# Performance work log

Measured on AMD Instinct MI355X. Metric: run time of the kernel, lower is better.

Reference implementation:

```python
import jax, jax.numpy as jnp
import numpy as np

MODEL_DIM = 1024
NUM_HEADS = 16
HEAD_DIM = MODEL_DIM // NUM_HEADS
BATCH = 2
SEQ = 2048


def setup_inputs() -> dict:
    key = jax.random.key(0)
    k1, k2, k3 = jax.random.split(key, 3)
    scale = 1.0 / np.sqrt(MODEL_DIM)
    return {
        "embeddings": jax.random.normal(k1, (BATCH, SEQ, MODEL_DIM), dtype=jnp.float32),
        "w_qkv": jax.random.normal(k2, (MODEL_DIM, 3 * MODEL_DIM), dtype=jnp.float32) * scale,
        "b_qkv": jnp.zeros((3 * MODEL_DIM,), dtype=jnp.float32),
        "w_out": jax.random.normal(k3, (MODEL_DIM, MODEL_DIM), dtype=jnp.float32) * scale,
        "b_out": jnp.zeros((MODEL_DIM,), dtype=jnp.float32),
    }


def reference(embeddings, w_qkv, b_qkv, w_out, b_out):
    B, S, _ = embeddings.shape
    # fused QKV projection: [B, S, 3*model_dim]
    qkv = embeddings @ w_qkv + b_qkv
    # -> [B, H, S, 3*head_dim], then split
    qkv = qkv.reshape(B, S, NUM_HEADS, 3 * HEAD_DIM).transpose(0, 2, 1, 3)
    q, k, v = jnp.split(qkv, 3, axis=-1)
    # scaled dot-product attention (full O(S^2) matrix, as in original)
    scale = 1.0 / jnp.sqrt(jnp.asarray(HEAD_DIM, dtype=embeddings.dtype))
    scores = jnp.einsum("bhqd,bhkd->bhqk", q, k) * scale
    attn = jax.nn.softmax(scores, axis=-1)
    ctx = jnp.einsum("bhqk,bhkd->bhqd", attn, v)
    # merge heads -> [B, S, model_dim], output projection
    ctx = ctx.transpose(0, 2, 1, 3).reshape(B, S, NUM_HEADS * HEAD_DIM)
    return ctx @ w_out + b_out
```

## Files before the change

kernel.cpp:

```cpp
#include <hip/hip_runtime.h>
#include <hip/hip_bf16.h>

#define MODEL 1024
#define NHEADS 16
#define HDIM 64
#define BATCH 2
#define SEQ 2048
#define NROWS (BATCH*SEQ)
#define QKVN (3*MODEL)
#define QSCALE 0.1803368801111204f

typedef __bf16 bf16x8 __attribute__((ext_vector_type(8)));
typedef float f32x4 __attribute__((ext_vector_type(4)));
typedef float f32x16 __attribute__((ext_vector_type(16)));

#define GLDS(g, l) __builtin_amdgcn_global_load_lds( \
    (const __attribute__((address_space(1))) void*)(g), \
    (__attribute__((address_space(3))) void*)(l), 16, 0, 0)

__device__ inline unsigned cvtpk(float lo, float hi) {
    unsigned r;
    asm("v_cvt_pk_bf16_f32 %0, %1, %2" : "=v"(r) : "v"(lo), "v"(hi));
    return r;
}

__device__ inline size_t qk_fidx(int s, int d) {
    return (((size_t)((s >> 6) * 8 + ((s >> 5) & 1) * 4 + (d >> 4)) * 64)
            + (s & 31) + ((d >> 3) & 1) * 32) * 8 + (d & 7);
}
__device__ inline size_t v_fidx(int s, int d) {
    return (((size_t)((s >> 6) * 8 + (d >> 5) * 4 + ((s >> 4) & 3)) * 64)
            + (d & 31) + ((s >> 3) & 1) * 32) * 8 + (s & 7);
}


__global__ __launch_bounds__(256) void prep_kernel(
    const float* __restrict__ emb, __hip_bfloat16* __restrict__ Xb,
    const float* __restrict__ wqkv, __hip_bfloat16* __restrict__ Wqkvt,
    const float* __restrict__ wout, __hip_bfloat16* __restrict__ Woutt)
{
    __shared__ float tile[32][33];
    int bid = blockIdx.x, tid = threadIdx.x;
    if (bid < 4096) {
        int i = (bid * 256 + tid) * 4;
        float4 v = *(const float4*)(emb + i);
        Xb[i + 0] = __float2bfloat16(v.x);
        Xb[i + 1] = __float2bfloat16(v.y);
        Xb[i + 2] = __float2bfloat16(v.z);
        Xb[i + 3] = __float2bfloat16(v.w);
        return;
    }
    const float* in; __hip_bfloat16* out; int K, N, n0, k0;
    if (bid < 7168) {
        int t = bid - 4096; in = wqkv; out = Wqkvt; K = MODEL; N = QKVN;
        n0 = (t % 96) * 32; k0 = (t / 96) * 32;
    } else {
        int t = bid - 7168; in = wout; out = Woutt; K = MODEL; N = MODEL;
        n0 = (t & 31) * 32; k0 = (t >> 5) * 32;
    }
    int tx = tid & 31, ty = tid >> 5;
#pragma unroll
    for (int i = 0; i < 4; ++i)
        tile[ty + i * 8][tx] = in[(size_t)(k0 + ty + i * 8) * N + n0 + tx];
    __syncthreads();
#pragma unroll
    for (int i = 0; i < 4; ++i)
        out[(size_t)(n0 + ty + i * 8) * K + k0 + tx] = __float2bfloat16(tile[tx][ty + i * 8]);
}


template<int EPI>
__global__ __launch_bounds__(256) void gemm_bt_kernel(
    const __hip_bfloat16* __restrict__ A, const __hip_bfloat16* __restrict__ Bt,
    const float* __restrict__ bias, float* __restrict__ Cf,
    __hip_bfloat16* __restrict__ qb, __hip_bfloat16* __restrict__ kb,
    __hip_bfloat16* __restrict__ vb, int M, int N, int K)
{
    __shared__ __hip_bfloat16 As[128 * 32];
    __shared__ __hip_bfloat16 Bs[128 * 32];
    int tid = threadIdx.x;
    int lane = tid & 63, wv = tid >> 6;
    int wm = wv >> 1, wn = wv & 1;
    int g = lane >> 4, li = lane & 15;
    int row0 = blockIdx.y * 128, col0 = blockIdx.x * 128;

    f32x4 acc[4][4] = {};

    for (int kt = 0; kt < K; kt += 32) {
        __syncthreads();
#pragma unroll
        for (int s = 0; s < 2; ++s) {
            int idx = (s * 256 + tid) * 8;
            int r = idx >> 5, c = idx & 31;
            const __hip_bfloat16* ga = A + (size_t)(row0 + r) * K + kt + c;
            char* la = (char*)As + (size_t)(s * 4 + wv) * 1024;
            GLDS(ga, la);
            const __hip_bfloat16* gb = Bt + (size_t)(col0 + r) * K + kt + c;
            char* lb = (char*)Bs + (size_t)(s * 4 + wv) * 1024;
            GLDS(gb, lb);
        }
        __syncthreads();
        bf16x8 a[4], b[4];
#pragma unroll
        for (int m = 0; m < 4; ++m)
            a[m] = *(const bf16x8*)((const char*)As + (size_t)((wm * 64 + m * 16 + li) * 32 + g * 8) * 2);
#pragma unroll
        for (int n = 0; n < 4; ++n)
            b[n] = *(const bf16x8*)((const char*)Bs + (size_t)((wn * 64 + n * 16 + li) * 32 + g * 8) * 2);
#pragma unroll
        for (int m = 0; m < 4; ++m)
#pragma unroll
            for (int n = 0; n < 4; ++n)
                acc[m][n] = __builtin_amdgcn_mfma_f32_16x16x32_bf16(a[m], b[n], acc[m][n], 0, 0, 0);
    }

    if (EPI == 1) {
#pragma unroll
        for (int m = 0; m < 4; ++m) {
            int row = row0 + wm * 64 + m * 16 + g * 4;
#pragma unroll
            for (int n = 0; n < 4; ++n) {
                int col = col0 + wn * 64 + n * 16 + li;
                float bv = bias[col];
#pragma unroll
                for (int r = 0; r < 4; ++r)
                    Cf[(size_t)(row + r) * N + col] = acc[m][n][r] + bv;
            }
        }
    } else {
#pragma unroll
        for (int m = 0; m < 4; ++m)
#pragma unroll
            for (int r = 0; r < 4; ++r) {
                int row = row0 + wm * 64 + m * 16 + g * 4 + r;
                int b = row >> 11, s = row & 2047;
#pragma unroll
                for (int n = 0; n < 4; ++n) {
                    int col = col0 + wn * 64 + n * 16 + li;
                    float val = acc[m][n][r] + bias[col];
                    int h = col / 192;
                    int rem = col - h * 192;
                    int t = rem >> 6, d = rem & 63;
                    size_t base = (size_t)(b * NHEADS + h) * (SEQ * HDIM);
                    if (t == 0)
                        qb[base + qk_fidx(s, d)] = __float2bfloat16(val * QSCALE);
                    else if (t == 1)
                        kb[base + qk_fidx(s, d)] = __float2bfloat16(val);
                    else
                        vb[base + v_fidx(s, d)] = __float2bfloat16(val);
                }
            }
    }
}


__global__ __launch_bounds__(256, 4) void attn_kernel(
    const __hip_bfloat16* __restrict__ qfb, const __hip_bfloat16* __restrict__ kfb,
    const __hip_bfloat16* __restrict__ vfb, __hip_bfloat16* __restrict__ ctx)
{
    __shared__ float Ms[2][64], Ls[2][64], Os[2][32][64];
    int tid = threadIdx.x;
    int lane = tid & 63, w = tid >> 6;
    int qg = w & 1, kvh = w >> 1;
    int qi = lane & 31, hi = lane >> 5;
    int bh = blockIdx.x;
    int b = bh >> 4, h = bh & 15;
    int q0 = blockIdx.y * 64 + qg * 32;

    const bf16x8* QF = (const bf16x8*)qfb + (size_t)bh * 16384;
    const bf16x8* KF = (const bf16x8*)kfb + (size_t)bh * 16384;
    const bf16x8* VF = (const bf16x8*)vfb + (size_t)bh * 16384;

    bf16x8 qv[4];
#pragma unroll
    for (int st = 0; st < 4; ++st)
        qv[st] = QF[(size_t)blockIdx.y * 512 + (qg * 4 + st) * 64 + lane];

    f32x16 o0 = {}, o1 = {};
    float m = -INFINITY, l = 0.f;

    bf16x8 kc[4], kn[4];
    {
        int t32 = kvh * 32, t64 = t32 >> 1, rh = t32 & 1;
#pragma unroll
        for (int st = 0; st < 4; ++st)
            kc[st] = KF[(size_t)t64 * 512 + (rh * 4 + st) * 64 + lane];
    }

    for (int tt = 0; tt < 32; ++tt) {
        int t32 = kvh * 32 + tt;
        int t64 = t32 >> 1, rh = t32 & 1;
        __builtin_amdgcn_s_barrier();

        f32x16 s = {};
#pragma unroll
        for (int st = 0; st < 4; ++st)
            s = __builtin_amdgcn_mfma_f32_32x32x16_bf16(kc[st], qv[st], s, 0, 0, 0);

        bf16x8 vv[4];
#pragma unroll
        for (int dr = 0; dr < 2; ++dr)
#pragma unroll
            for (int ksl = 0; ksl < 2; ++ksl)
                vv[dr * 2 + ksl] = VF[(size_t)t64 * 512 + (dr * 4 + rh * 2 + ksl) * 64 + lane];
        {
            int tp = (tt < 31) ? t32 + 1 : t32;
            int p64 = tp >> 1, ph = tp & 1;
#pragma unroll
            for (int st = 0; st < 4; ++st)
                kn[st] = KF[(size_t)p64 * 512 + (ph * 4 + st) * 64 + lane];
        }

        float tm[8];
#pragma unroll
        for (int i = 0; i < 8; ++i) tm[i] = fmaxf(s[i], s[8 + i]);
#pragma unroll
        for (int i = 0; i < 4; ++i) tm[i] = fmaxf(tm[i], tm[4 + i]);
        float mx = fmaxf(fmaxf(tm[0], tm[1]), fmaxf(tm[2], tm[3]));
        mx = fmaxf(mx, __shfl_xor(mx, 32));
        if (__any(mx - m > 8.0f)) {
            float mn = fmaxf(m, mx);
            float al = __builtin_amdgcn_exp2f(m - mn);
            m = mn;
            l *= al;
#pragma unroll
            for (int i = 0; i < 16; ++i) { o0[i] *= al; o1[i] *= al; }
        }
#pragma unroll
        for (int i = 0; i < 16; ++i) s[i] = __builtin_amdgcn_exp2f(s[i] - m);
        float ts[8];
#pragma unroll
        for (int i = 0; i < 8; ++i) ts[i] = s[i] + s[8 + i];
#pragma unroll
        for (int i = 0; i < 4; ++i) ts[i] = ts[i] + ts[4 + i];
        float sum = (ts[0] + ts[1]) + (ts[2] + ts[3]);
        sum += __shfl_xor(sum, 32);
        l += sum;

        bf16x8 pb[2];
#pragma unroll
        for (int ksl = 0; ksl < 2; ++ksl) {
            const int base = ksl * 8;
            unsigned t0 = cvtpk(s[base + 0], s[base + 1]);
            unsigned t1 = cvtpk(s[base + 2], s[base + 3]);
            unsigned u0 = cvtpk(s[base + 4], s[base + 5]);
            unsigned u1 = cvtpk(s[base + 6], s[base + 7]);
            unsigned ra = __shfl_xor(hi ? t0 : u0, 32);
            unsigned rb = __shfl_xor(hi ? t1 : u1, 32);
            union { unsigned u[4]; bf16x8 v; } pk;
            pk.u[0] = hi ? ra : t0;
            pk.u[1] = hi ? rb : t1;
            pk.u[2] = hi ? u0 : ra;
            pk.u[3] = hi ? u1 : rb;
            pb[ksl] = pk.v;
        }

        o0 = __builtin_amdgcn_mfma_f32_32x32x16_bf16(vv[0], pb[0], o0, 0, 0, 0);
        o0 = __builtin_amdgcn_mfma_f32_32x32x16_bf16(vv[1], pb[1], o0, 0, 0, 0);
        o1 = __builtin_amdgcn_mfma_f32_32x32x16_bf16(vv[2], pb[0], o1, 0, 0, 0);
        o1 = __builtin_amdgcn_mfma_f32_32x32x16_bf16(vv[3], pb[1], o1, 0, 0, 0);

#pragma unroll
        for (int st = 0; st < 4; ++st) kc[st] = kn[st];
    }

    __syncthreads();
    if (kvh == 1) {
        Ms[qg][lane] = m; Ls[qg][lane] = l;
#pragma unroll
        for (int i = 0; i < 16; ++i) { Os[qg][i][lane] = o0[i]; Os[qg][16 + i][lane] = o1[i]; }
    }
    __syncthreads();
    if (kvh == 0) {
        float m2 = Ms[qg][lane], l2 = Ls[qg][lane];
        float mn = fmaxf(m, m2);
        float a = __builtin_amdgcn_exp2f(m - mn);
        float b2 = __builtin_amdgcn_exp2f(m2 - mn);
        float linv = 1.f / (l * a + l2 * b2);
        __hip_bfloat16* crow = ctx + ((size_t)(b * SEQ) + q0 + qi) * MODEL + h * HDIM;
#pragma unroll
        for (int rg = 0; rg < 4; ++rg) {
            float c0[4], c1[4];
#pragma unroll
            for (int e = 0; e < 4; ++e) {
                int i = rg * 4 + e;
                c0[e] = (o0[i] * a + Os[qg][i][lane] * b2) * linv;
                c1[e] = (o1[i] * a + Os[qg][16 + i][lane] * b2) * linv;
            }
            uint2 pk0, pk1;
            pk0.x = cvtpk(c0[0], c0[1]); pk0.y = cvtpk(c0[2], c0[3]);
            pk1.x = cvtpk(c1[0], c1[1]); pk1.y = cvtpk(c1[2], c1[3]);
            *(uint2*)(crow + rg * 8 + hi * 4) = pk0;
            *(uint2*)(crow + 32 + rg * 8 + hi * 4) = pk1;
        }
    }
}


extern "C" void kernel_launch(void* const* d_in, const int* in_sizes, int n_in,
                              void* d_out, int out_size, void* d_ws, size_t ws_size,
                              hipStream_t stream) {
    const float* emb = (const float*)d_in[0];
    const float* w_qkv = (const float*)d_in[1];
    const float* b_qkv = (const float*)d_in[2];
    const float* w_out = (const float*)d_in[3];
    const float* b_out = (const float*)d_in[4];
    float* out = (float*)d_out;
    char* ws = (char*)d_ws;

    __hip_bfloat16* Xb    = (__hip_bfloat16*)(ws);
    __hip_bfloat16* Wqkvt = (__hip_bfloat16*)(ws + ((size_t)8  << 20));
    __hip_bfloat16* Woutt = (__hip_bfloat16*)(ws + ((size_t)14 << 20));
    __hip_bfloat16* qbuf  = (__hip_bfloat16*)(ws + ((size_t)16 << 20));
    __hip_bfloat16* kbuf  = (__hip_bfloat16*)(ws + ((size_t)24 << 20));
    __hip_bfloat16* vbuf  = (__hip_bfloat16*)(ws + ((size_t)32 << 20));
    __hip_bfloat16* ctx   = (__hip_bfloat16*)(ws + ((size_t)40 << 20));

    prep_kernel<<<8192, 256, 0, stream>>>(emb, Xb, w_qkv, Wqkvt, w_out, Woutt);

    gemm_bt_kernel<0><<<dim3(QKVN / 128, NROWS / 128), 256, 0, stream>>>(
        Xb, Wqkvt, b_qkv, nullptr, qbuf, kbuf, vbuf, NROWS, QKVN, MODEL);

    attn_kernel<<<dim3(BATCH * NHEADS, SEQ / 64), 256, 0, stream>>>(qbuf, kbuf, vbuf, ctx);

    gemm_bt_kernel<1><<<dim3(MODEL / 128, NROWS / 128), 256, 0, stream>>>(
        ctx, Woutt, b_out, out, nullptr, nullptr, nullptr, NROWS, MODEL, MODEL);
}
```

Before: 206.8 us.

## Double GEMM K-tile, hoist QKV scatter indexing, defer softmax sum shuffle

The bf16 GEMM now stages a 64-wide K slice per iteration instead of 32, which halves the number of barrier pairs and issues two MFMAs per accumulator per tile, at the cost of twice the LDS per block. The QKV epilogue splits the fragment-index math into separable row and column parts and hoists the per-column destination pointer, scale and bias out of the row loop, removing per-element divides and branches. In attention, the cross-half row-sum shuffle is moved out of the KV loop and done once at the end, which relies on the rescale factor being uniform across the two half-waves.

```diff
diff --git a/kernel.cpp b/kernel.cpp
--- a/kernel.cpp
+++ b/kernel.cpp
@@ -24,14 +24,10 @@
     return r;
 }
 
-__device__ inline size_t qk_fidx(int s, int d) {
-    return (((size_t)((s >> 6) * 8 + ((s >> 5) & 1) * 4 + (d >> 4)) * 64)
-            + (s & 31) + ((d >> 3) & 1) * 32) * 8 + (d & 7);
-}
-__device__ inline size_t v_fidx(int s, int d) {
-    return (((size_t)((s >> 6) * 8 + (d >> 5) * 4 + ((s >> 4) & 3)) * 64)
-            + (d & 31) + ((s >> 3) & 1) * 32) * 8 + (s & 7);
-}
+__device__ inline int qk_fs(int s) { return ((s >> 6) << 12) + (((s >> 5) & 1) << 11) + ((s & 31) << 3); }
+__device__ inline int qk_fd(int d) { return ((d >> 4) << 9) + (((d >> 3) & 1) << 8) + (d & 7); }
+__device__ inline int v_fs(int s) { return ((s >> 6) << 12) + (((s >> 4) & 3) << 9) + (((s >> 3) & 1) << 8) + (s & 7); }
+__device__ inline int v_fd(int d) { return ((d >> 5) << 11) + ((d & 31) << 3); }
 
 
 __global__ __launch_bounds__(256) void prep_kernel(
@@ -76,8 +72,8 @@
     __hip_bfloat16* __restrict__ qb, __hip_bfloat16* __restrict__ kb,
     __hip_bfloat16* __restrict__ vb, int M, int N, int K)
 {
-    __shared__ __hip_bfloat16 As[128 * 32];
-    __shared__ __hip_bfloat16 Bs[128 * 32];
+    __shared__ __hip_bfloat16 As[128 * 64];
+    __shared__ __hip_bfloat16 Bs[128 * 64];
     int tid = threadIdx.x;
     int lane = tid & 63, wv = tid >> 6;
     int wm = wv >> 1, wn = wv & 1;
@@ -86,32 +82,33 @@
 
     f32x4 acc[4][4] = {};
 
-    for (int kt = 0; kt < K; kt += 32) {
+    for (int kt = 0; kt < K; kt += 64) {
         __syncthreads();
 #pragma unroll
-        for (int s = 0; s < 2; ++s) {
-            int idx = (s * 256 + tid) * 8;
-            int r = idx >> 5, c = idx & 31;
-            const __hip_bfloat16* ga = A + (size_t)(row0 + r) * K + kt + c;
-            char* la = (char*)As + (size_t)(s * 4 + wv) * 1024;
-            GLDS(ga, la);
-            const __hip_bfloat16* gb = Bt + (size_t)(col0 + r) * K + kt + c;
-            char* lb = (char*)Bs + (size_t)(s * 4 + wv) * 1024;
-            GLDS(gb, lb);
+        for (int s4 = 0; s4 < 4; ++s4) {
+            int idx = (s4 * 256 + tid) * 8;
+            int r = idx >> 6, c = idx & 63;
+            GLDS(A + (size_t)(row0 + r) * K + kt + c, (char*)As + (size_t)(s4 * 4 + wv) * 1024);
+            GLDS(Bt + (size_t)(col0 + r) * K + kt + c, (char*)Bs + (size_t)(s4 * 4 + wv) * 1024);
         }
         __syncthreads();
-        bf16x8 a[4], b[4];
+        bf16x8 a[2][4], b[2][4];
+#pragma unroll
+        for (int kk = 0; kk < 2; ++kk) {
+#pragma unroll
+            for (int m = 0; m < 4; ++m)
+                a[kk][m] = *(const bf16x8*)((const char*)As + (size_t)(((wm * 64 + m * 16 + li) * 64 + kk * 32 + g * 8) * 2));
+#pragma unroll
+            for (int n = 0; n < 4; ++n)
+                b[kk][n] = *(const bf16x8*)((const char*)Bs + (size_t)(((wn * 64 + n * 16 + li) * 64 + kk * 32 + g * 8) * 2));
+        }
 #pragma unroll
         for (int m = 0; m < 4; ++m)
-            a[m] = *(const bf16x8*)((const char*)As + (size_t)((wm * 64 + m * 16 + li) * 32 + g * 8) * 2);
-#pragma unroll
-        for (int n = 0; n < 4; ++n)
-            b[n] = *(const bf16x8*)((const char*)Bs + (size_t)((wn * 64 + n * 16 + li) * 32 + g * 8) * 2);
-#pragma unroll
-        for (int m = 0; m < 4; ++m)
-#pragma unroll
-            for (int n = 0; n < 4; ++n)
-                acc[m][n] = __builtin_amdgcn_mfma_f32_16x16x32_bf16(a[m], b[n], acc[m][n], 0, 0, 0);
+#pragma unroll
+            for (int n = 0; n < 4; ++n) {
+                acc[m][n] = __builtin_amdgcn_mfma_f32_16x16x32_bf16(a[0][m], b[0][n], acc[m][n], 0, 0, 0);
+                acc[m][n] = __builtin_amdgcn_mfma_f32_16x16x32_bf16(a[1][m], b[1][n], acc[m][n], 0, 0, 0);
+            }
     }
 
     if (EPI == 1) {
@@ -128,26 +125,34 @@
             }
         }
     } else {
+        __hip_bfloat16* dstn[4];
+        float bvn[4], qmn[4];
+        int tpn[4];
+#pragma unroll
+        for (int n = 0; n < 4; ++n) {
+            int col = col0 + wn * 64 + n * 16 + li;
+            int h = col / 192;
+            int rem = col - h * 192;
+            int t = rem >> 6, d = rem & 63;
+            tpn[n] = t;
+            qmn[n] = (t == 0) ? QSCALE : 1.0f;
+            bvn[n] = bias[col];
+            __hip_bfloat16* base = (t == 0) ? qb : ((t == 1) ? kb : vb);
+            dstn[n] = base + (size_t)h * (SEQ * HDIM) + ((t == 2) ? v_fd(d) : qk_fd(d));
+        }
 #pragma unroll
         for (int m = 0; m < 4; ++m)
 #pragma unroll
             for (int r = 0; r < 4; ++r) {
                 int row = row0 + wm * 64 + m * 16 + g * 4 + r;
-                int b = row >> 11, s = row & 2047;
+                int s = row & 2047;
+                int bofs = (row >> 11) * (NHEADS * SEQ * HDIM);
+                int fsqk = qk_fs(s), fsv = v_fs(s);
 #pragma unroll
                 for (int n = 0; n < 4; ++n) {
-                    int col = col0 + wn * 64 + n * 16 + li;
-                    float val = acc[m][n][r] + bias[col];
-                    int h = col / 192;
-                    int rem = col - h * 192;
-                    int t = rem >> 6, d = rem & 63;
-                    size_t base = (size_t)(b * NHEADS + h) * (SEQ * HDIM);
-                    if (t == 0)
-                        qb[base + qk_fidx(s, d)] = __float2bfloat16(val * QSCALE);
-                    else if (t == 1)
-                        kb[base + qk_fidx(s, d)] = __float2bfloat16(val);
-                    else
-                        vb[base + v_fidx(s, d)] = __float2bfloat16(val);
+                    float val = (acc[m][n][r] + bvn[n]) * qmn[n];
+                    int off = bofs + ((tpn[n] == 2) ? fsv : fsqk);
+                    dstn[n][off] = __float2bfloat16(val);
                 }
             }
     }
@@ -234,7 +239,6 @@
 #pragma unroll
         for (int i = 0; i < 4; ++i) ts[i] = ts[i] + ts[4 + i];
         float sum = (ts[0] + ts[1]) + (ts[2] + ts[3]);
-        sum += __shfl_xor(sum, 32);
         l += sum;
 
         bf16x8 pb[2];
@@ -264,6 +268,8 @@
         for (int st = 0; st < 4; ++st) kc[st] = kn[st];
     }
 
+    l += __shfl_xor(l, 32);
+
     __syncthreads();
     if (kvh == 1) {
         Ms[qg][lane] = m; Ls[qg][lane] = l;
```

Result: slower. 211.7 us (+2.4%).
